# Kernel optimization log

Measured on AMD Instinct MI355X. Metric: run time of the kernel, lower is better.

Reference implementation:

```python
import jax, jax.numpy as jnp
import numpy as np

CODEBOOK_DIM = 256
HIDDEN_DIM = 512
OUT_CHANNELS = 1
NUM_NODES = 16384
NUM_INPUT_ROWS = 12288


def setup_inputs() -> dict:
    key = jax.random.key(0)
    k0, k1, k2, k3, k4 = jax.random.split(key, 5)
    x = jax.random.normal(k0, (NUM_INPUT_ROWS, CODEBOOK_DIM), dtype=jnp.float32)
    # GCNConv params: linear weight (no bias in lin) + additive bias after aggregation
    W1 = jax.random.normal(k1, (CODEBOOK_DIM, HIDDEN_DIM), dtype=jnp.float32) * (1.0 / np.sqrt(CODEBOOK_DIM))
    b1 = jax.random.normal(k2, (HIDDEN_DIM,), dtype=jnp.float32) * 0.01
    W2 = jax.random.normal(k3, (HIDDEN_DIM, OUT_CHANNELS), dtype=jnp.float32) * (1.0 / np.sqrt(HIDDEN_DIM))
    b2 = jax.random.normal(k4, (OUT_CHANNELS,), dtype=jnp.float32) * 0.01
    return {"x": x, "W1": W1, "b1": b1, "W2": W2, "b2": b2, "num_nodes": NUM_NODES}


def _gcn_complete(h, W, b, n):
    # GCNConv on a complete graph (no self-loop edges in edge_index, but
    # GCNConv adds self-loops): A_hat = D^{-1/2}(A+I)D^{-1/2} = J/N since
    # A+I is all-ones and every degree is N. So aggregation == column mean
    # broadcast to every node.
    hw = h @ W                                   # [N, d_out]
    agg = jnp.mean(hw, axis=0, keepdims=True)    # [1, d_out]
    return jnp.broadcast_to(agg, (n, W.shape[1])) + b


def reference(x, W1, b1, W2, b2, num_nodes):
    n = num_nodes
    missing = n - x.shape[0]
    x = jnp.concatenate([x, jnp.zeros((missing, x.shape[1]), x.dtype)], axis=0)  # [N, codebook_dim]
    h = jax.nn.relu(_gcn_complete(x, W1, b1, n))   # [N, hidden]
    out = jax.nn.relu(_gcn_complete(h, W2, b2, n)) # [N, out_channels]
    return out
```

## Files before the change

### kernel.cpp

```cpp
#include <hip/hip_runtime.h>

#define NROWS   12288
#define NCOLS   256
#define HID     512
#define NNODES  16384

__global__ __launch_bounds__(256) void colsum_partial(const float* __restrict__ x,
                                                      float* __restrict__ wsA,
                                                      int nblocks) {
    const int t    = threadIdx.x;
    const int c4   = t & 63;
    const int rofs = t >> 6;
    const int bid  = blockIdx.x;
    const float4* __restrict__ x4 = (const float4*)x;

    float4 acc = make_float4(0.f, 0.f, 0.f, 0.f);
    for (int r = bid * 4 + rofs; r < NROWS; r += 4 * nblocks) {
        float4 v = x4[r * 64 + c4];
        acc.x += v.x; acc.y += v.y; acc.z += v.z; acc.w += v.w;
    }

    __shared__ float4 s[256];
    s[t] = acc;
    __syncthreads();
    if (t < 64) {
        float4 a = s[t], b = s[t + 64], c = s[t + 128], d = s[t + 192];
        float4 r;
        r.x = a.x + b.x + c.x + d.x;
        r.y = a.y + b.y + c.y + d.y;
        r.z = a.z + b.z + c.z + d.z;
        r.w = a.w + b.w + c.w + d.w;
        ((float4*)wsA)[bid * 64 + t] = r;
    }
}

__global__ __launch_bounds__(512) void hidden_kernel(const float* __restrict__ wsA,
                                                     const float* __restrict__ W1,
                                                     const float* __restrict__ b1,
                                                     const float* __restrict__ W2,
                                                     float* __restrict__ wsB,
                                                     int nb) {
    __shared__ float4 colmean4[NCOLS / 4];
    __shared__ float4 tmp4[512];
    __shared__ float  part[512];

    const int t = threadIdx.x;
    const int b = blockIdx.x;

    {
        const int c4  = t & 63;
        const int grp = t >> 6;
        const int per = nb >> 3;
        const float4* __restrict__ wsA4 = (const float4*)wsA;

        float4 acc = make_float4(0.f, 0.f, 0.f, 0.f);
        const int k0 = grp * per;
        #pragma unroll 4
        for (int k = k0; k < k0 + per; ++k) {
            float4 v = wsA4[k * 64 + c4];
            acc.x += v.x; acc.y += v.y; acc.z += v.z; acc.w += v.w;
        }
        tmp4[t] = acc;
        __syncthreads();
        if (t < 64) {
            float4 a = tmp4[t];
            #pragma unroll
            for (int g = 1; g < 8; ++g) {
                float4 v = tmp4[g * 64 + t];
                a.x += v.x; a.y += v.y; a.z += v.z; a.w += v.w;
            }
            const float inv = 1.0f / (float)NNODES;
            a.x *= inv; a.y *= inv; a.z *= inv; a.w *= inv;
            colmean4[t] = a;
        }
        __syncthreads();
    }

    const float* __restrict__ colmean = (const float*)colmean4;
    const int w   = t >> 6;
    const int l   = t & 63;
    const int myt = b * 64 + l;

    float pa = 0.f;
    const int cbase = w * 32;
    #pragma unroll
    for (int c = cbase; c < cbase + 32; ++c)
        pa = fmaf(colmean[c], W1[c * HID + myt], pa);
    part[t] = pa;
    __syncthreads();

    if (t < 64) {
        float hs = b1[myt];
        #pragma unroll
        for (int g = 0; g < 8; ++g)
            hs += part[g * 64 + l];
        const float h = fmaxf(hs, 0.0f);

        float p = h * W2[myt];
        #pragma unroll
        for (int off = 32; off > 0; off >>= 1)
            p += __shfl_down(p, off, 64);
        if (l == 0) wsB[b] = p;
    }
}

__global__ __launch_bounds__(256) void broadcast_kernel(const float* __restrict__ wsB,
                                                        const float* __restrict__ b2,
                                                        float* __restrict__ out) {
    __shared__ float sval;
    if (threadIdx.x == 0) {
        float s = b2[0];
        #pragma unroll
        for (int i = 0; i < 8; ++i) s += wsB[i];
        sval = fmaxf(s, 0.0f);
    }
    __syncthreads();
    const float v = sval;
    float4 f4 = make_float4(v, v, v, v);
    ((float4*)out)[blockIdx.x * 256 + threadIdx.x] = f4;
}

extern "C" void kernel_launch(void* const* d_in, const int* in_sizes, int n_in,
                              void* d_out, int out_size, void* d_ws, size_t ws_size,
                              hipStream_t stream) {
    const float* x  = (const float*)d_in[0];
    const float* W1 = (const float*)d_in[1];
    const float* b1 = (const float*)d_in[2];
    const float* W2 = (const float*)d_in[3];
    const float* b2 = (const float*)d_in[4];
    float* out = (float*)d_out;
    float* ws  = (float*)d_ws;

    int nb = 128;
    {
        size_t need = (size_t)nb * NCOLS * sizeof(float) + 8 * sizeof(float);
        if (ws_size < need) {
            nb = (int)((ws_size - 8 * sizeof(float)) / (NCOLS * sizeof(float)));
            nb &= ~7;
            if (nb < 8) nb = 8;
        }
    }
    float* wsA = ws;
    float* wsB = ws + (size_t)nb * NCOLS;

    colsum_partial<<<nb, 256, 0, stream>>>(x, wsA, nb);
    hidden_kernel<<<8, 512, 0, stream>>>(wsA, W1, b1, W2, wsB, nb);
    broadcast_kernel<<<16, 256, 0, stream>>>(wsB, b2, out);
}
```

Before: 15.47 us.

## Fuse hidden and broadcast kernels into one redundant-compute tail kernel

Merges the hidden-layer matvec and the output broadcast into a single kernel launched on 16 blocks. Each block recomputes the column means, the full 512-wide hidden vector and the scalar output, then writes its slice of the output. This removes one kernel launch and the workspace round-trip, at the cost of 16x redundant reads of W1 and of the partial sums. The first-stage block count is also doubled from 128 to 256.

Measured after the change: 18.57 us. 1.2x slower.

```diff
diff --git a/kernel.cpp b/kernel.cpp
--- a/kernel.cpp
+++ b/kernel.cpp
@@ -34,18 +34,19 @@
     }
 }
 
-__global__ __launch_bounds__(512) void hidden_kernel(const float* __restrict__ wsA,
-                                                     const float* __restrict__ W1,
-                                                     const float* __restrict__ b1,
-                                                     const float* __restrict__ W2,
-                                                     float* __restrict__ wsB,
-                                                     int nb) {
-    __shared__ float4 colmean4[NCOLS / 4];
+__global__ __launch_bounds__(512) void fused_tail(const float* __restrict__ wsA,
+                                                  const float* __restrict__ W1,
+                                                  const float* __restrict__ b1,
+                                                  const float* __restrict__ W2,
+                                                  const float* __restrict__ b2,
+                                                  float* __restrict__ out,
+                                                  int nb) {
     __shared__ float4 tmp4[512];
-    __shared__ float  part[512];
+    __shared__ float  colmean[NCOLS];
+    __shared__ float  warpsums[8];
+    __shared__ float  s_scalar;
 
     const int t = threadIdx.x;
-    const int b = blockIdx.x;
 
     {
         const int c4  = t & 63;
@@ -71,53 +72,40 @@
             }
             const float inv = 1.0f / (float)NNODES;
             a.x *= inv; a.y *= inv; a.z *= inv; a.w *= inv;
-            colmean4[t] = a;
+            ((float4*)colmean)[t] = a;
         }
         __syncthreads();
     }
 
-    const float* __restrict__ colmean = (const float*)colmean4;
-    const int w   = t >> 6;
-    const int l   = t & 63;
-    const int myt = b * 64 + l;
+    float a0 = 0.f, a1 = 0.f, a2 = 0.f, a3 = 0.f;
+    #pragma unroll 4
+    for (int c = 0; c < NCOLS; c += 4) {
+        a0 = fmaf(colmean[c + 0], W1[(c + 0) * HID + t], a0);
+        a1 = fmaf(colmean[c + 1], W1[(c + 1) * HID + t], a1);
+        a2 = fmaf(colmean[c + 2], W1[(c + 2) * HID + t], a2);
+        a3 = fmaf(colmean[c + 3], W1[(c + 3) * HID + t], a3);
+    }
+    const float h = fmaxf(b1[t] + ((a0 + a1) + (a2 + a3)), 0.0f);
 
-    float pa = 0.f;
-    const int cbase = w * 32;
+    float p = h * W2[t];
     #pragma unroll
-    for (int c = cbase; c < cbase + 32; ++c)
-        pa = fmaf(colmean[c], W1[c * HID + myt], pa);
-    part[t] = pa;
+    for (int off = 32; off > 0; off >>= 1)
+        p += __shfl_down(p, off, 64);
+    if ((t & 63) == 0) warpsums[t >> 6] = p;
+    __syncthreads();
+    if (t == 0) {
+        float s = b2[0];
+        #pragma unroll
+        for (int w = 0; w < 8; ++w) s += warpsums[w];
+        s_scalar = fmaxf(s, 0.0f);
+    }
     __syncthreads();
 
-    if (t < 64) {
-        float hs = b1[myt];
-        #pragma unroll
-        for (int g = 0; g < 8; ++g)
-            hs += part[g * 64 + l];
-        const float h = fmaxf(hs, 0.0f);
-
-        float p = h * W2[myt];
-        #pragma unroll
-        for (int off = 32; off > 0; off >>= 1)
-            p += __shfl_down(p, off, 64);
-        if (l == 0) wsB[b] = p;
+    const float v = s_scalar;
+    if (t < 256) {
+        float4 f4 = make_float4(v, v, v, v);
+        ((float4*)out)[blockIdx.x * 256 + t] = f4;
     }
-}
-
-__global__ __launch_bounds__(256) void broadcast_kernel(const float* __restrict__ wsB,
-                                                        const float* __restrict__ b2,
-                                                        float* __restrict__ out) {
-    __shared__ float sval;
-    if (threadIdx.x == 0) {
-        float s = b2[0];
-        #pragma unroll
-        for (int i = 0; i < 8; ++i) s += wsB[i];
-        sval = fmaxf(s, 0.0f);
-    }
-    __syncthreads();
-    const float v = sval;
-    float4 f4 = make_float4(v, v, v, v);
-    ((float4*)out)[blockIdx.x * 256 + threadIdx.x] = f4;
 }
 
 extern "C" void kernel_launch(void* const* d_in, const int* in_sizes, int n_in,
@@ -129,21 +117,18 @@
     const float* W2 = (const float*)d_in[3];
     const float* b2 = (const float*)d_in[4];
     float* out = (float*)d_out;
-    float* ws  = (float*)d_ws;
+    float* wsA = (float*)d_ws;
 
-    int nb = 128;
+    int nb = 256;
     {
-        size_t need = (size_t)nb * NCOLS * sizeof(float) + 8 * sizeof(float);
+        size_t need = (size_t)nb * NCOLS * sizeof(float);
         if (ws_size < need) {
-            nb = (int)((ws_size - 8 * sizeof(float)) / (NCOLS * sizeof(float)));
+            nb = (int)(ws_size / (NCOLS * sizeof(float)));
             nb &= ~7;
             if (nb < 8) nb = 8;
         }
     }
-    float* wsA = ws;
-    float* wsB = ws + (size_t)nb * NCOLS;
 
     colsum_partial<<<nb, 256, 0, stream>>>(x, wsA, nb);
-    hidden_kernel<<<8, 512, 0, stream>>>(wsA, W1, b1, W2, wsB, nb);
-    broadcast_kernel<<<16, 256, 0, stream>>>(wsB, b2, out);
+    fused_tail<<<16, 512, 0, stream>>>(wsA, W1, b1, W2, b2, out, nb);
 }
```

## Fuse hidden and broadcast kernels using an atomic counter grid barrier

Applied to the files above, without the earlier changes.

Merges the hidden-layer kernel and the output broadcast kernel into one launch of 8 blocks. Each block publishes its partial dot product atomically and bumps a counter, then spins until all 8 blocks are done before summing and writing its slice of the output. The counter is reset by the first kernel. This removes one kernel launch and its gap, but relies on all 8 blocks being co-resident and adds spin-wait latency.

Measured after the change: 17.86 us. 1.15x slower.

```diff
diff --git a/kernel.cpp b/kernel.cpp
--- a/kernel.cpp
+++ b/kernel.cpp
@@ -4,16 +4,21 @@
 #define NCOLS   256
 #define HID     512
 #define NNODES  16384
+#define TB      8
+
 
 __global__ __launch_bounds__(256) void colsum_partial(const float* __restrict__ x,
                                                       float* __restrict__ wsA,
+                                                      unsigned int* __restrict__ cnt,
                                                       int nblocks) {
     const int t    = threadIdx.x;
     const int c4   = t & 63;
     const int rofs = t >> 6;
     const int bid  = blockIdx.x;
+
+    if (bid == 0 && t == 0) *cnt = 0u;
+
     const float4* __restrict__ x4 = (const float4*)x;
-
     float4 acc = make_float4(0.f, 0.f, 0.f, 0.f);
     for (int r = bid * 4 + rofs; r < NROWS; r += 4 * nblocks) {
         float4 v = x4[r * 64 + c4];
@@ -34,15 +39,19 @@
     }
 }
 
-__global__ __launch_bounds__(512) void hidden_kernel(const float* __restrict__ wsA,
-                                                     const float* __restrict__ W1,
-                                                     const float* __restrict__ b1,
-                                                     const float* __restrict__ W2,
-                                                     float* __restrict__ wsB,
-                                                     int nb) {
-    __shared__ float4 colmean4[NCOLS / 4];
+__global__ __launch_bounds__(512) void fused_tail(const float* __restrict__ wsA,
+                                                  const float* __restrict__ W1,
+                                                  const float* __restrict__ b1,
+                                                  const float* __restrict__ W2,
+                                                  const float* __restrict__ b2,
+                                                  float* __restrict__ ws2,
+                                                  unsigned int* __restrict__ cnt,
+                                                  float* __restrict__ out,
+                                                  int nb) {
     __shared__ float4 tmp4[512];
+    __shared__ float  colmean[NCOLS];
     __shared__ float  part[512];
+    __shared__ float  s_bcast;
 
     const int t = threadIdx.x;
     const int b = blockIdx.x;
@@ -71,53 +80,56 @@
             }
             const float inv = 1.0f / (float)NNODES;
             a.x *= inv; a.y *= inv; a.z *= inv; a.w *= inv;
-            colmean4[t] = a;
+            ((float4*)colmean)[t] = a;
         }
         __syncthreads();
     }
 
-    const float* __restrict__ colmean = (const float*)colmean4;
-    const int w   = t >> 6;
-    const int l   = t & 63;
-    const int myt = b * 64 + l;
+    {
+        const int w   = t >> 6;
+        const int l   = t & 63;
+        const int myt = b * 64 + l;
 
-    float pa = 0.f;
-    const int cbase = w * 32;
-    #pragma unroll
-    for (int c = cbase; c < cbase + 32; ++c)
-        pa = fmaf(colmean[c], W1[c * HID + myt], pa);
-    part[t] = pa;
+        float pa = 0.f;
+        const int cbase = w * 32;
+        #pragma unroll
+        for (int c = cbase; c < cbase + 32; ++c)
+            pa = fmaf(colmean[c], W1[c * HID + myt], pa);
+        part[t] = pa;
+        __syncthreads();
+
+        if (t < 64) {
+            float hs = b1[myt];
+            #pragma unroll
+            for (int g = 0; g < 8; ++g)
+                hs += part[g * 64 + l];
+            const float h = fmaxf(hs, 0.0f);
+
+            float p = h * W2[myt];
+            #pragma unroll
+            for (int off = 32; off > 0; off >>= 1)
+                p += __shfl_down(p, off, 64);
+            if (l == 0) {
+                atomicExch(&ws2[b], p);
+                __threadfence();
+                atomicAdd(cnt, 1u);
+            }
+        }
+    }
+
+    if (t == 0) {
+        while (atomicAdd(cnt, 0u) < (unsigned)TB)
+            __builtin_amdgcn_s_sleep(8);
+        float s = b2[0];
+        #pragma unroll
+        for (int i = 0; i < TB; ++i)
+            s += atomicAdd(&ws2[i], 0.0f);
+        s_bcast = fmaxf(s, 0.0f);
+    }
     __syncthreads();
 
-    if (t < 64) {
-        float hs = b1[myt];
-        #pragma unroll
-        for (int g = 0; g < 8; ++g)
-            hs += part[g * 64 + l];
-        const float h = fmaxf(hs, 0.0f);
-
-        float p = h * W2[myt];
-        #pragma unroll
-        for (int off = 32; off > 0; off >>= 1)
-            p += __shfl_down(p, off, 64);
-        if (l == 0) wsB[b] = p;
-    }
-}
-
-__global__ __launch_bounds__(256) void broadcast_kernel(const float* __restrict__ wsB,
-                                                        const float* __restrict__ b2,
-                                                        float* __restrict__ out) {
-    __shared__ float sval;
-    if (threadIdx.x == 0) {
-        float s = b2[0];
-        #pragma unroll
-        for (int i = 0; i < 8; ++i) s += wsB[i];
-        sval = fmaxf(s, 0.0f);
-    }
-    __syncthreads();
-    const float v = sval;
-    float4 f4 = make_float4(v, v, v, v);
-    ((float4*)out)[blockIdx.x * 256 + threadIdx.x] = f4;
+    const float v = s_bcast;
+    ((float4*)out)[b * 512 + t] = make_float4(v, v, v, v);
 }
 
 extern "C" void kernel_launch(void* const* d_in, const int* in_sizes, int n_in,
@@ -133,17 +145,17 @@
 
     int nb = 128;
     {
-        size_t need = (size_t)nb * NCOLS * sizeof(float) + 8 * sizeof(float);
+        size_t need = ((size_t)nb * NCOLS + TB + 1) * sizeof(float);
         if (ws_size < need) {
-            nb = (int)((ws_size - 8 * sizeof(float)) / (NCOLS * sizeof(float)));
+            nb = (int)((ws_size / sizeof(float) - (TB + 1)) / NCOLS);
             nb &= ~7;
             if (nb < 8) nb = 8;
         }
     }
-    float* wsA = ws;
-    float* wsB = ws + (size_t)nb * NCOLS;
+    float*        wsA = ws;
+    float*        ws2 = ws + (size_t)nb * NCOLS;
+    unsigned int* cnt = (unsigned int*)(ws2 + TB);
 
-    colsum_partial<<<nb, 256, 0, stream>>>(x, wsA, nb);
-    hidden_kernel<<<8, 512, 0, stream>>>(wsA, W1, b1, W2, wsB, nb);
-    broadcast_kernel<<<16, 256, 0, stream>>>(wsB, b2, out);
+    colsum_partial<<<nb, 256, 0, stream>>>(x, wsA, cnt, nb);
+    fused_tail<<<TB, 512, 0, stream>>>(wsA, W1, b1, W2, b2, ws2, cnt, out, nb);
 }
```
